# Kernel tuning notes

Hardware: AMD Instinct MI355X
Metric: run time of the kernel (lower is better)

Reference implementation:

```python
import jax, jax.numpy as jnp
import numpy as np

B, V, N, H, C_OUT = 16, 8192, 2048, 128, 7


def setup_inputs() -> dict:
    key = jax.random.key(0)
    ks = jax.random.split(key, 5)
    return {
        "verts": jax.random.normal(ks[0], (B, V, 3), jnp.float32) * 10.0,
        "coords_ca": jax.random.normal(ks[1], (B, N, 3), jnp.float32) * 10.0,
        "feats": jax.random.normal(ks[2], (B, N, H), jnp.float32),
        "W1": jax.random.normal(ks[3], (H, H), jnp.float32) / np.sqrt(H),
        "b1": jnp.zeros((H,), jnp.float32),
        "W2": jax.random.normal(ks[4], (H, C_OUT), jnp.float32) / np.sqrt(H),
        "b2": jnp.zeros((C_OUT,), jnp.float32),
    }


def reference(verts, coords_ca, feats, W1, b1, W2, b2):
    # Per-graph: nearest-CA match for every surface vertex (cdist + argmin),
    # then sum over the UNIQUE set of matched residues (torch: processed[min_indices.unique()].sum(-2)).
    # Equivalent jit-friendly form: hit-mask over residues, masked sum.
    def per_graph(v, c, f):
        # squared euclidean distances [V, N]; argmin is invariant to the sqrt
        d = (jnp.sum(v * v, -1)[:, None]
             - 2.0 * (v @ c.T)
             + jnp.sum(c * c, -1)[None, :])
        mi = jnp.argmin(d, axis=1)                       # [V] nearest residue per vertex
        hit = jnp.zeros((c.shape[0],), f.dtype).at[mi].add(1.0)
        mask = (hit > 0).astype(f.dtype)                 # [N] residue selected at least once
        return jnp.einsum('nh,n->h', f, mask)            # sum over unique selected residues

    pooled = jax.vmap(per_graph)(verts, coords_ca, feats)  # [B, H]
    # top_net (Dropout is identity in eval)
    h = jax.nn.relu(pooled @ W1 + b1)
    return h @ W2 + b2                                    # [B, 7]
```

## Files before the change

### kernel.cpp

```cpp
#include <hip/hip_runtime.h>
#include <hip/hip_bf16.h>

#define B_GR   16
#define V_PTS  8192
#define N_RES  2048
#define H_DIM  128
#define C_OUT  7
#define SEGS   16

#define NSPLIT 16
#define NL     (N_RES / NSPLIT)
#define VPT    4
#define VBLK   (256 * VPT)
#define VBLKS  (V_PTS / VBLK)

__global__ __launch_bounds__(256, 8) void k_argmin(const float* __restrict__ verts,
                                                   const float* __restrict__ coords,
                                                   unsigned long long* __restrict__ mi64) {
    __shared__ float4 sc[NL];
    const int b  = blockIdx.x / (VBLKS * NSPLIT);
    const int r  = blockIdx.x % (VBLKS * NSPLIT);
    const int vb = r / NSPLIT;
    const int ns = r % NSPLIT;

    const float* cbase = coords + ((size_t)b * N_RES + ns * NL) * 3;
    if (threadIdx.x < NL) {
        const int i = threadIdx.x;
        float x = cbase[i * 3 + 0];
        float y = cbase[i * 3 + 1];
        float z = cbase[i * 3 + 2];
        float csq = __fadd_rn(__fadd_rn(__fmul_rn(x, x), __fmul_rn(y, y)), __fmul_rn(z, z));
        sc[i] = make_float4(x, y, z, csq);
    }
    __syncthreads();

    const int vbase = vb * VBLK + threadIdx.x;
    const float* vp = verts + (size_t)b * V_PTS * 3;

    float vx[VPT], vy[VPT], vz[VPT], vsq[VPT], best[VPT];
    int bi[VPT];
#pragma unroll
    for (int k = 0; k < VPT; ++k) {
        const int v = vbase + k * 256;
        vx[k] = vp[v * 3 + 0];
        vy[k] = vp[v * 3 + 1];
        vz[k] = vp[v * 3 + 2];
        vsq[k] = __fadd_rn(__fadd_rn(__fmul_rn(vx[k], vx[k]), __fmul_rn(vy[k], vy[k])),
                           __fmul_rn(vz[k], vz[k]));
        best[k] = 3.402823466e+38f;
        bi[k] = 0;
    }

#pragma unroll 4
    for (int n = 0; n < NL; ++n) {
        const float4 c = sc[n];
#pragma unroll
        for (int k = 0; k < VPT; ++k) {
            float dot = __fadd_rn(__fadd_rn(__fmul_rn(vx[k], c.x), __fmul_rn(vy[k], c.y)),
                                  __fmul_rn(vz[k], c.z));
            float d = __fadd_rn(fmaf(-2.0f, dot, vsq[k]), c.w);
            bool m = d < best[k];
            best[k] = m ? d : best[k];
            bi[k]   = m ? n : bi[k];
        }
    }

#pragma unroll
    for (int k = 0; k < VPT; ++k) {
        unsigned int bits = __float_as_uint(best[k]);
        unsigned int key  = bits ^ (unsigned int)(((int)bits >> 31) | 0x80000000);
        unsigned long long packed =
            ((unsigned long long)key << 32) | (unsigned int)(ns * NL + bi[k]);
        atomicMin(&mi64[(size_t)b * V_PTS + vbase + k * 256], packed);
    }
}

__global__ __launch_bounds__(256) void k_pool(const unsigned long long* __restrict__ mi64,
                                              const float* __restrict__ feats,
                                              float* __restrict__ partial) {
    __shared__ float msk[N_RES];
    __shared__ float4 red[8][32];
    const int b   = blockIdx.x >> 4;
    const int seg = blockIdx.x & (SEGS - 1);

    for (int i = threadIdx.x; i < N_RES; i += 256) msk[i] = 0.0f;
    __syncthreads();

    const unsigned long long* mb = mi64 + (size_t)b * V_PTS;
    for (int v = threadIdx.x; v < V_PTS; v += 256)
        msk[(unsigned int)mb[v]] = 1.0f;
    __syncthreads();

    const int q = threadIdx.x & 31;
    const int s = threadIdx.x >> 5;
    const int n0 = seg * (N_RES / SEGS);
    const float4* fb4 = (const float4*)(feats + ((size_t)b * N_RES + n0) * H_DIM);

    float4 acc = make_float4(0.f, 0.f, 0.f, 0.f);
#pragma unroll
    for (int n = 0; n < N_RES / SEGS / 8; ++n) {
        const int nn = s + n * 8;
        const float m = msk[n0 + nn];
        const float4 f = fb4[(size_t)nn * 32 + q];
        acc.x = fmaf(f.x, m, acc.x);
        acc.y = fmaf(f.y, m, acc.y);
        acc.z = fmaf(f.z, m, acc.z);
        acc.w = fmaf(f.w, m, acc.w);
    }
    red[s][q] = acc;
    __syncthreads();

    if (s == 0) {
        float4 t = acc;
#pragma unroll
        for (int i = 1; i < 8; ++i) {
            t.x += red[i][q].x; t.y += red[i][q].y;
            t.z += red[i][q].z; t.w += red[i][q].w;
        }
        ((float4*)partial)[((size_t)b * SEGS + seg) * 32 + q] = t;
    }
}

__global__ __launch_bounds__(128) void k_mlp(const float* __restrict__ partial,
                                             const float* __restrict__ W1,
                                             const float* __restrict__ b1,
                                             const float* __restrict__ W2,
                                             const float* __restrict__ b2,
                                             float* __restrict__ out) {
    __shared__ float pooled[H_DIM];
    __shared__ float h1[H_DIM];
    const int b = blockIdx.x;
    const int j = threadIdx.x;

    float s = 0.0f;
#pragma unroll
    for (int g = 0; g < SEGS; ++g)
        s += partial[((size_t)b * SEGS + g) * H_DIM + j];
    pooled[j] = s;
    __syncthreads();

    float acc = b1[j];
#pragma unroll 8
    for (int hh = 0; hh < H_DIM; ++hh)
        acc = fmaf(pooled[hh], W1[hh * H_DIM + j], acc);
    h1[j] = fmaxf(acc, 0.0f);
    __syncthreads();

    if (j < C_OUT) {
        float o = b2[j];
#pragma unroll 8
        for (int hh = 0; hh < H_DIM; ++hh)
            o = fmaf(h1[hh], W2[hh * C_OUT + j], o);
        out[(size_t)b * C_OUT + j] = o;
    }
}

extern "C" void kernel_launch(void* const* d_in, const int* in_sizes, int n_in,
                              void* d_out, int out_size, void* d_ws, size_t ws_size,
                              hipStream_t stream) {
    const float* verts  = (const float*)d_in[0];
    const float* coords = (const float*)d_in[1];
    const float* feats  = (const float*)d_in[2];
    const float* W1     = (const float*)d_in[3];
    const float* b1     = (const float*)d_in[4];
    const float* W2     = (const float*)d_in[5];
    const float* b2     = (const float*)d_in[6];
    float* out = (float*)d_out;

    unsigned long long* mi64 = (unsigned long long*)d_ws;
    float* partial = (float*)((char*)d_ws + (size_t)B_GR * V_PTS * 8);

    hipMemsetAsync(mi64, 0xFF, (size_t)B_GR * V_PTS * 8, stream);
    k_argmin<<<B_GR * VBLKS * NSPLIT, 256, 0, stream>>>(verts, coords, mi64);
    k_pool  <<<B_GR * SEGS,           256, 0, stream>>>(mi64, feats, partial);
    k_mlp   <<<B_GR,                  128, 0, stream>>>(partial, W1, b1, W2, b2, out);
}
```

Baseline: 152.2 us.

## Replace brute-force nearest-residue search with x-bucketed sorted slab search

Adds a prep kernel that counting-sorts residues by x coordinate into 512 buckets, then a search kernel that seeds a best distance from 32 nearby sorted residues and scans only the x-slab that could hold a closer point. Hit marks are written directly into a residue mask, which removes the packed atomicMin buffer and its memset. This cuts the O(V·N) distance work to roughly the slab size per vertex. The bucket range [-52,52] is hardcoded, but buckets are clamped, so correctness should hold for any input. The old brute-force path remains as a fallback when the workspace is too small, with more vertices per thread.

```diff
diff --git a/kernel.cpp b/kernel.cpp
--- a/kernel.cpp
+++ b/kernel.cpp
@@ -7,19 +7,176 @@
 #define H_DIM  128
 #define C_OUT  7
 #define SEGS   16
+#define NB     512
+#define CPAD   520
+
+
+__device__ __forceinline__ int bucketof(float x) {
+    int bk = (int)floorf((x + 52.0f) * (512.0f / 104.0f));
+    return bk < 0 ? 0 : (bk > NB - 1 ? NB - 1 : bk);
+}
+
+__device__ __forceinline__ void eval_one(const float4 c, int id,
+                                         float vx, float vy, float vz, float vsq,
+                                         float& best, int& bidx) {
+    float dot = __fadd_rn(__fadd_rn(__fmul_rn(vx, c.x), __fmul_rn(vy, c.y)),
+                          __fmul_rn(vz, c.z));
+    float d = __fadd_rn(fmaf(-2.0f, dot, vsq), c.w);
+    bool take = (d < best) || ((d == best) && (id < bidx));
+    best = take ? d : best;
+    bidx = take ? id : bidx;
+}
+
+__global__ __launch_bounds__(256) void k_prep(const float* __restrict__ coords,
+                                              float4* __restrict__ sf4g,
+                                              unsigned int* __restrict__ sidxg,
+                                              unsigned int* __restrict__ cellsg,
+                                              float* __restrict__ msk) {
+    __shared__ unsigned int hist[NB];
+    __shared__ unsigned int sA[NB], sB[NB];
+    __shared__ unsigned int cursor[NB];
+    const int b = blockIdx.x;
+    const int tid = threadIdx.x;
+
+    for (int i = tid; i < NB; i += 256) hist[i] = 0;
+    for (int i = tid; i < N_RES; i += 256) msk[b * N_RES + i] = 0.0f;
+    __syncthreads();
+
+    const float* cb = coords + (size_t)b * N_RES * 3;
+    for (int i = tid; i < N_RES; i += 256)
+        atomicAdd(&hist[bucketof(cb[i * 3])], 1u);
+    __syncthreads();
+
+    for (int i = tid; i < NB; i += 256) sA[i] = hist[i];
+    __syncthreads();
+    unsigned int* src = sA;
+    unsigned int* dst = sB;
+    for (int off = 1; off < NB; off <<= 1) {
+        for (int i = tid; i < NB; i += 256)
+            dst[i] = src[i] + (i >= off ? src[i - off] : 0u);
+        __syncthreads();
+        unsigned int* t = src; src = dst; dst = t;
+    }
+    for (int i = tid; i < NB; i += 256) {
+        unsigned int ex = src[i] - hist[i];
+        cellsg[b * CPAD + i] = ex;
+        cursor[i] = ex;
+    }
+    if (tid == 0) cellsg[b * CPAD + NB] = N_RES;
+    __syncthreads();
+
+    for (int i = tid; i < N_RES; i += 256) {
+        float x = cb[i * 3 + 0];
+        float y = cb[i * 3 + 1];
+        float z = cb[i * 3 + 2];
+        float csq = __fadd_rn(__fadd_rn(__fmul_rn(x, x), __fmul_rn(y, y)), __fmul_rn(z, z));
+        unsigned int pos = atomicAdd(&cursor[bucketof(x)], 1u);
+        sf4g[(size_t)b * N_RES + pos] = make_float4(x, y, z, csq);
+        sidxg[(size_t)b * N_RES + pos] = (unsigned int)i;
+    }
+}
+
+__global__ __launch_bounds__(256) void k_search(const float* __restrict__ verts,
+                                                const float4* __restrict__ sf4g,
+                                                const unsigned int* __restrict__ sidxg,
+                                                const unsigned int* __restrict__ cellsg,
+                                                float* __restrict__ msk) {
+    __shared__ float4 sf4[N_RES];
+    __shared__ unsigned short sidx[N_RES];
+    __shared__ unsigned short cs[NB + 1];
+    const int b     = blockIdx.x >> 5;
+    const int chunk = blockIdx.x & 31;
+
+    for (int i = threadIdx.x; i < N_RES; i += 256) {
+        sf4[i]  = sf4g[(size_t)b * N_RES + i];
+        sidx[i] = (unsigned short)sidxg[(size_t)b * N_RES + i];
+    }
+    for (int i = threadIdx.x; i < NB + 1; i += 256)
+        cs[i] = (unsigned short)cellsg[b * CPAD + i];
+    __syncthreads();
+
+    const int v = chunk * 256 + threadIdx.x;
+    const float* vp = verts + ((size_t)b * V_PTS + v) * 3;
+    const float vx = vp[0], vy = vp[1], vz = vp[2];
+    const float vsq = __fadd_rn(__fadd_rn(__fmul_rn(vx, vx), __fmul_rn(vy, vy)),
+                                __fmul_rn(vz, vz));
+
+    float best = 3.402823466e+38f;
+    int bidx = 1 << 30;
+
+    {
+        int j0 = cs[bucketof(vx)];
+        int lo = j0 - 16;
+        lo = lo < 0 ? 0 : (lo > N_RES - 32 ? N_RES - 32 : lo);
+#pragma unroll 4
+        for (int j = lo; j < lo + 32; ++j)
+            eval_one(sf4[j], (int)sidx[j], vx, vy, vz, vsq, best, bidx);
+    }
+
+    const float W = sqrtf(best + 1.0f) + 0.0625f;
+    const int bklo = bucketof(vx - W);
+    const int bkhi = bucketof(vx + W);
+    const int jlo = cs[bklo];
+    const int jhi = cs[bkhi + 1];
+#pragma unroll 4
+    for (int j = jlo; j < jhi; ++j)
+        eval_one(sf4[j], (int)sidx[j], vx, vy, vz, vsq, best, bidx);
+
+    msk[b * N_RES + bidx] = 1.0f;
+}
+
+__global__ __launch_bounds__(256) void k_pool_m(const float* __restrict__ msk,
+                                                const float* __restrict__ feats,
+                                                float* __restrict__ partial) {
+    __shared__ float sm[N_RES / SEGS];
+    __shared__ float4 red[8][32];
+    const int b   = blockIdx.x >> 4;
+    const int seg = blockIdx.x & (SEGS - 1);
+    const int n0  = seg * (N_RES / SEGS);
+
+    if (threadIdx.x < N_RES / SEGS) sm[threadIdx.x] = msk[b * N_RES + n0 + threadIdx.x];
+    __syncthreads();
+
+    const int q = threadIdx.x & 31;
+    const int s = threadIdx.x >> 5;
+    const float4* fb4 = (const float4*)(feats + ((size_t)b * N_RES + n0) * H_DIM);
+
+    float4 acc = make_float4(0.f, 0.f, 0.f, 0.f);
+#pragma unroll
+    for (int n = 0; n < N_RES / SEGS / 8; ++n) {
+        const int nn = s + n * 8;
+        const float m = sm[nn];
+        const float4 f = fb4[(size_t)nn * 32 + q];
+        acc.x = fmaf(f.x, m, acc.x);
+        acc.y = fmaf(f.y, m, acc.y);
+        acc.z = fmaf(f.z, m, acc.z);
+        acc.w = fmaf(f.w, m, acc.w);
+    }
+    red[s][q] = acc;
+    __syncthreads();
+
+    if (s == 0) {
+        float4 t = acc;
+#pragma unroll
+        for (int i = 1; i < 8; ++i) {
+            t.x += red[i][q].x; t.y += red[i][q].y;
+            t.z += red[i][q].z; t.w += red[i][q].w;
+        }
+        ((float4*)partial)[((size_t)b * SEGS + seg) * 32 + q] = t;
+    }
+}
 
 #define NSPLIT 16
 #define NL     (N_RES / NSPLIT)
-#define VPT    4
-#define VBLK   (256 * VPT)
-#define VBLKS  (V_PTS / VBLK)
-
-__global__ __launch_bounds__(256, 8) void k_argmin(const float* __restrict__ verts,
-                                                   const float* __restrict__ coords,
-                                                   unsigned long long* __restrict__ mi64) {
+#define FVPT   8
+#define FVBLK  (256 * FVPT)
+#define FVBLKS (V_PTS / FVBLK)
+__global__ __launch_bounds__(256, 4) void k_argmin_at(const float* __restrict__ verts,
+                                                      const float* __restrict__ coords,
+                                                      unsigned long long* __restrict__ mi64) {
     __shared__ float4 sc[NL];
-    const int b  = blockIdx.x / (VBLKS * NSPLIT);
-    const int r  = blockIdx.x % (VBLKS * NSPLIT);
+    const int b  = blockIdx.x / (FVBLKS * NSPLIT);
+    const int r  = blockIdx.x % (FVBLKS * NSPLIT);
     const int vb = r / NSPLIT;
     const int ns = r % NSPLIT;
 
@@ -34,13 +191,13 @@
     }
     __syncthreads();
 
-    const int vbase = vb * VBLK + threadIdx.x;
+    const int vbase = vb * FVBLK + threadIdx.x;
     const float* vp = verts + (size_t)b * V_PTS * 3;
 
-    float vx[VPT], vy[VPT], vz[VPT], vsq[VPT], best[VPT];
-    int bi[VPT];
-#pragma unroll
-    for (int k = 0; k < VPT; ++k) {
+    float vx[FVPT], vy[FVPT], vz[FVPT], vsq[FVPT], best[FVPT];
+    int bi[FVPT];
+#pragma unroll
+    for (int k = 0; k < FVPT; ++k) {
         const int v = vbase + k * 256;
         vx[k] = vp[v * 3 + 0];
         vy[k] = vp[v * 3 + 1];
@@ -50,12 +207,11 @@
         best[k] = 3.402823466e+38f;
         bi[k] = 0;
     }
-
-#pragma unroll 4
+#pragma unroll 2
     for (int n = 0; n < NL; ++n) {
         const float4 c = sc[n];
 #pragma unroll
-        for (int k = 0; k < VPT; ++k) {
+        for (int k = 0; k < FVPT; ++k) {
             float dot = __fadd_rn(__fadd_rn(__fmul_rn(vx[k], c.x), __fmul_rn(vy[k], c.y)),
                                   __fmul_rn(vz[k], c.z));
             float d = __fadd_rn(fmaf(-2.0f, dot, vsq[k]), c.w);
@@ -64,9 +220,8 @@
             bi[k]   = m ? n : bi[k];
         }
     }
-
-#pragma unroll
-    for (int k = 0; k < VPT; ++k) {
+#pragma unroll
+    for (int k = 0; k < FVPT; ++k) {
         unsigned int bits = __float_as_uint(best[k]);
         unsigned int key  = bits ^ (unsigned int)(((int)bits >> 31) | 0x80000000);
         unsigned long long packed =
@@ -75,9 +230,9 @@
     }
 }
 
-__global__ __launch_bounds__(256) void k_pool(const unsigned long long* __restrict__ mi64,
-                                              const float* __restrict__ feats,
-                                              float* __restrict__ partial) {
+__global__ __launch_bounds__(256) void k_pool_at(const unsigned long long* __restrict__ mi64,
+                                                 const float* __restrict__ feats,
+                                                 float* __restrict__ partial) {
     __shared__ float msk[N_RES];
     __shared__ float4 red[8][32];
     const int b   = blockIdx.x >> 4;
@@ -85,7 +240,6 @@
 
     for (int i = threadIdx.x; i < N_RES; i += 256) msk[i] = 0.0f;
     __syncthreads();
-
     const unsigned long long* mb = mi64 + (size_t)b * V_PTS;
     for (int v = threadIdx.x; v < V_PTS; v += 256)
         msk[(unsigned int)mb[v]] = 1.0f;
@@ -109,7 +263,6 @@
     }
     red[s][q] = acc;
     __syncthreads();
-
     if (s == 0) {
         float4 t = acc;
 #pragma unroll
@@ -167,11 +320,31 @@
     const float* b2     = (const float*)d_in[6];
     float* out = (float*)d_out;
 
-    unsigned long long* mi64 = (unsigned long long*)d_ws;
-    float* partial = (float*)((char*)d_ws + (size_t)B_GR * V_PTS * 8);
-
-    hipMemsetAsync(mi64, 0xFF, (size_t)B_GR * V_PTS * 8, stream);
-    k_argmin<<<B_GR * VBLKS * NSPLIT, 256, 0, stream>>>(verts, coords, mi64);
-    k_pool  <<<B_GR * SEGS,           256, 0, stream>>>(mi64, feats, partial);
-    k_mlp   <<<B_GR,                  128, 0, stream>>>(partial, W1, b1, W2, b2, out);
-}
+    const size_t sf4_bytes  = (size_t)B_GR * N_RES * 16;
+    const size_t sidx_bytes = (size_t)B_GR * N_RES * 4;
+    const size_t cell_bytes = (size_t)B_GR * CPAD * 4;
+    const size_t msk_bytes  = (size_t)B_GR * N_RES * 4;
+    const size_t pp_bytes   = (size_t)B_GR * SEGS * H_DIM * 4;
+    const size_t need = sf4_bytes + sidx_bytes + cell_bytes + msk_bytes + pp_bytes;
+
+    if (ws_size >= need) {
+        float4*       sf4g  = (float4*)d_ws;
+        unsigned int* sidxg = (unsigned int*)((char*)d_ws + sf4_bytes);
+        unsigned int* cells = (unsigned int*)((char*)d_ws + sf4_bytes + sidx_bytes);
+        float* msk     = (float*)((char*)d_ws + sf4_bytes + sidx_bytes + cell_bytes);
+        float* partial = (float*)((char*)d_ws + sf4_bytes + sidx_bytes + cell_bytes + msk_bytes);
+
+        k_prep  <<<B_GR,              256, 0, stream>>>(coords, sf4g, sidxg, cells, msk);
+        k_search<<<B_GR * V_PTS / 256, 256, 0, stream>>>(verts, sf4g, sidxg, cells, msk);
+        k_pool_m<<<B_GR * SEGS,       256, 0, stream>>>(msk, feats, partial);
+        k_mlp   <<<B_GR,              128, 0, stream>>>(partial, W1, b1, W2, b2, out);
+    } else {
+        unsigned long long* mi64 = (unsigned long long*)d_ws;
+        float* partial = (float*)((char*)d_ws + (size_t)B_GR * V_PTS * 8);
+
+        hipMemsetAsync(mi64, 0xFF, (size_t)B_GR * V_PTS * 8, stream);
+        k_argmin_at<<<B_GR * FVBLKS * NSPLIT, 256, 0, stream>>>(verts, coords, mi64);
+        k_pool_at  <<<B_GR * SEGS,            256, 0, stream>>>(mi64, feats, partial);
+        k_mlp      <<<B_GR,                   128, 0, stream>>>(partial, W1, b1, W2, b2, out);
+    }
+}
```

Result: slower. 321.4 us (+111.3%).
